# Kernel tuning notes

Measured on AMD Instinct MI355X. Metric: run time of the kernel, lower is better.

The kernel has to match this reference:

```python
import jax, jax.numpy as jnp
import numpy as np

KERNEL_SIZE = 5
SIGMA = 1.5
SIGMA_COLOR = 0.1
EPS = 1e-8


def _gaussian_kernel_2d(k, sigma):
    x = jnp.arange(k, dtype=jnp.float32) - k // 2
    k1 = jnp.exp(-0.5 * (x / sigma) ** 2)
    k1 = k1 / k1.sum()
    return jnp.outer(k1, k1)  # [k, k]


def setup_inputs() -> dict:
    key = jax.random.key(0)
    img = jax.random.uniform(key, (2, 3, 1024, 1024), dtype=jnp.float32)
    return {"img": img}


def reference(img):
    # Bilateral filter, faithful to Denoise._bilateral_filter.
    B, C, H, W = img.shape
    k = KERNEL_SIZE
    pad = k // 2
    k2 = _gaussian_kernel_2d(k, SIGMA).astype(img.dtype).reshape(-1)  # [k*k]

    img_padded = jnp.pad(img, ((0, 0), (0, 0), (pad, pad), (pad, pad)), mode='reflect')
    # patches: [B, C, H, W, k*k] via k*k shifted views (loop over fixed small window)
    patches = jnp.stack(
        [img_padded[:, :, i:i + H, j:j + W] for i in range(k) for j in range(k)],
        axis=-1,
    )
    center = img[..., None]
    intensity_diff = patches - center
    color_weights = jnp.exp(-0.5 * (intensity_diff / SIGMA_COLOR) ** 2)
    weights = color_weights * k2  # broadcast spatial gaussian over last axis
    weights_sum = weights.sum(axis=-1, keepdims=True) + EPS
    weights_normalized = weights / weights_sum
    img_filtered = (patches * weights_normalized).sum(axis=-1)
    return img_filtered
```

## Files before the change

kernel.cpp:

```cpp
#include <hip/hip_runtime.h>


#define TX 64
#define TY 64
#define BY 4
#define RPT (TY / BY)
#define PAD 2
#define LW (TX + 2 * PAD)
#define LH (TY + 2 * PAD)

#if __has_builtin(__builtin_amdgcn_exp2f)
#define EXP2(x) __builtin_amdgcn_exp2f(x)
#else
#define EXP2(x) exp2f(x)
#endif

__global__ __launch_bounds__(256) void bilateral_kernel(
    const float* __restrict__ in, float* __restrict__ out, int H, int W)
{
    const int z  = blockIdx.z;
    const int x0 = blockIdx.x * TX;
    const int y0 = blockIdx.y * TY;
    const int tx = threadIdx.x;
    const int ty = threadIdx.y;
    const int tid = ty * TX + tx;

    __shared__ float tile[LH * LW];
    const float* img = in + (size_t)z * H * W;

    for (int idx = tid; idx < LH * LW; idx += TX * BY) {
        int r = idx / LW;
        int c = idx - r * LW;
        int gy = y0 - PAD + r;
        int gx = x0 - PAD + c;
        gy = gy < 0 ? -gy : (gy >= H ? 2 * H - 2 - gy : gy);
        gx = gx < 0 ? -gx : (gx >= W ? 2 * W - 2 - gx : gx);
        tile[idx] = img[(size_t)gy * W + gx];
    }
    __syncthreads();

    float k1[5];
    float s = 0.f;
#pragma unroll
    for (int i = 0; i < 5; ++i) {
        float x = (float)(i - 2) * (1.0f / 1.5f);
        k1[i] = __expf(-0.5f * x * x);
        s += k1[i];
    }
    const float inv_s = 1.0f / s;
    float l1[5];
#pragma unroll
    for (int i = 0; i < 5; ++i) l1[i] = __log2f(k1[i] * inv_s);
    float lk2[5][5];
#pragma unroll
    for (int i = 0; i < 5; ++i)
#pragma unroll
        for (int j = 0; j < 5; ++j) lk2[i][j] = l1[i] + l1[j];
    const float K2C = EXP2(lk2[2][2]);
    const float S = 8.49321794f;

    const int ly0 = ty * RPT;

    float win[5][5];
#pragma unroll
    for (int r = 0; r < 4; ++r)
#pragma unroll
        for (int j = 0; j < 5; ++j)
            win[r][j] = tile[(ly0 + r) * LW + tx + j];

#pragma unroll
    for (int q = 0; q < RPT; ++q) {
        const int fill = (q + 4) % 5;
#pragma unroll
        for (int j = 0; j < 5; ++j)
            win[fill][j] = tile[(ly0 + q + 4) * LW + tx + j];

        const float ctr = win[(q + 2) % 5][2];
        float wsum = K2C;
        float vsum = K2C * ctr;
#pragma unroll
        for (int i = 0; i < 5; ++i) {
            const int ri = (q + i) % 5;
#pragma unroll
            for (int j = 0; j < 5; ++j) {
                if (i == 2 && j == 2) continue;
                const float p = win[ri][j];
                const float u = (p - ctr) * S;
                const float w = EXP2(__builtin_fmaf(-u, u, lk2[i][j]));
                wsum += w;
                vsum = __builtin_fmaf(w, p, vsum);
            }
        }
        const float r = __builtin_amdgcn_rcpf(wsum + 1e-8f);
        out[((size_t)z * H + (y0 + ly0 + q)) * W + (x0 + tx)] = vsum * r;
    }
}

extern "C" void kernel_launch(void* const* d_in, const int* in_sizes, int n_in,
                              void* d_out, int out_size, void* d_ws, size_t ws_size,
                              hipStream_t stream) {
    const float* img = (const float*)d_in[0];
    float* out = (float*)d_out;

    const int B = 2, C = 3, H = 1024, W = 1024;
    dim3 block(TX, BY, 1);
    dim3 grid(W / TX, H / TY, B * C);
    bilateral_kernel<<<grid, block, 0, stream>>>(img, out, H, W);
}
```

Measured before the change: 106.5 us.

## Process two output rows per iteration with pre-scaled tile and constant spatial weights

Halves the tile height to launch more blocks, pre-multiplies the shared tile by the color scale so the per-tap subtract-multiply becomes a single subtract, hard-codes the log2 spatial kernel constants, and computes two output rows per loop step with split accumulators to raise ILP. The final normalization folds the scale back in through an FMA. The change costs more registers per thread and more halo reloads per output because of the shorter tiles. An unused constant-memory dummy variable is also added.

```diff
diff --git a/kernel.cpp b/kernel.cpp
--- a/kernel.cpp
+++ b/kernel.cpp
@@ -2,7 +2,7 @@
 
 
 #define TX 64
-#define TY 64
+#define TY 32
 #define BY 4
 #define RPT (TY / BY)
 #define PAD 2
@@ -15,6 +15,8 @@
 #define EXP2(x) exp2f(x)
 #endif
 
+__device__ __constant__ const float d_dummy = 0.f;
+
 __global__ __launch_bounds__(256) void bilateral_kernel(
     const float* __restrict__ in, float* __restrict__ out, int H, int W)
 {
@@ -24,6 +26,9 @@
     const int tx = threadIdx.x;
     const int ty = threadIdx.y;
     const int tid = ty * TX + tx;
+
+    const float S    = 8.49321794f;
+    const float SEPS = 8.49321794e-8f;
 
     __shared__ float tile[LH * LW];
     const float* img = in + (size_t)z * H * W;
@@ -35,33 +40,17 @@
         int gx = x0 - PAD + c;
         gy = gy < 0 ? -gy : (gy >= H ? 2 * H - 2 - gy : gy);
         gx = gx < 0 ? -gx : (gx >= W ? 2 * W - 2 - gx : gx);
-        tile[idx] = img[(size_t)gy * W + gx];
+        tile[idx] = img[(size_t)gy * W + gx] * S;
     }
     __syncthreads();
 
-    float k1[5];
-    float s = 0.f;
-#pragma unroll
-    for (int i = 0; i < 5; ++i) {
-        float x = (float)(i - 2) * (1.0f / 1.5f);
-        k1[i] = __expf(-0.5f * x * x);
-        s += k1[i];
-    }
-    const float inv_s = 1.0f / s;
-    float l1[5];
-#pragma unroll
-    for (int i = 0; i < 5; ++i) l1[i] = __log2f(k1[i] * inv_s);
-    float lk2[5][5];
-#pragma unroll
-    for (int i = 0; i < 5; ++i)
-#pragma unroll
-        for (int j = 0; j < 5; ++j) lk2[i][j] = l1[i] + l1[j];
-    const float K2C = EXP2(lk2[2][2]);
-    const float S = 8.49321794f;
+    const float L[5] = {-3.0579510f, -2.0961485f, -1.7755560f,
+                        -2.0961485f, -3.0579510f};
+    const float K2C = 0.08531170f;
 
     const int ly0 = ty * RPT;
 
-    float win[5][5];
+    float win[6][5];
 #pragma unroll
     for (int r = 0; r < 4; ++r)
 #pragma unroll
@@ -69,30 +58,51 @@
             win[r][j] = tile[(ly0 + r) * LW + tx + j];
 
 #pragma unroll
-    for (int q = 0; q < RPT; ++q) {
-        const int fill = (q + 4) % 5;
+    for (int q = 0; q < RPT; q += 2) {
+        const int sA = (q + 4) % 6, sB = (q + 5) % 6;
 #pragma unroll
         for (int j = 0; j < 5; ++j)
-            win[fill][j] = tile[(ly0 + q + 4) * LW + tx + j];
+            win[sA][j] = tile[(ly0 + q + 4) * LW + tx + j];
+#pragma unroll
+        for (int j = 0; j < 5; ++j)
+            win[sB][j] = tile[(ly0 + q + 5) * LW + tx + j];
 
-        const float ctr = win[(q + 2) % 5][2];
-        float wsum = K2C;
-        float vsum = K2C * ctr;
+        const float c0 = win[(q + 2) % 6][2];
+        const float c1 = win[(q + 3) % 6][2];
+
+        float w0a = K2C, v0a = K2C * c0, w0b = 0.f, v0b = 0.f;
+        float w1a = K2C, v1a = K2C * c1, w1b = 0.f, v1b = 0.f;
+
 #pragma unroll
         for (int i = 0; i < 5; ++i) {
-            const int ri = (q + i) % 5;
+            const int r0 = (q + i) % 6;
+            const int r1 = (q + 1 + i) % 6;
 #pragma unroll
             for (int j = 0; j < 5; ++j) {
-                if (i == 2 && j == 2) continue;
-                const float p = win[ri][j];
-                const float u = (p - ctr) * S;
-                const float w = EXP2(__builtin_fmaf(-u, u, lk2[i][j]));
-                wsum += w;
-                vsum = __builtin_fmaf(w, p, vsum);
+                const float lk2 = L[i] + L[j];
+                if (!(i == 2 && j == 2)) {
+                    const float p = win[r0][j];
+                    const float u = p - c0;
+                    const float w = EXP2(__builtin_fmaf(-u, u, lk2));
+                    if (((i * 5 + j) & 1) == 0) { w0a += w; v0a = __builtin_fmaf(w, p, v0a); }
+                    else                        { w0b += w; v0b = __builtin_fmaf(w, p, v0b); }
+                }
+                if (!(i == 2 && j == 2)) {
+                    const float p = win[r1][j];
+                    const float u = p - c1;
+                    const float w = EXP2(__builtin_fmaf(-u, u, lk2));
+                    if (((i * 5 + j) & 1) == 0) { w1a += w; v1a = __builtin_fmaf(w, p, v1a); }
+                    else                        { w1b += w; v1b = __builtin_fmaf(w, p, v1b); }
+                }
             }
         }
-        const float r = __builtin_amdgcn_rcpf(wsum + 1e-8f);
-        out[((size_t)z * H + (y0 + ly0 + q)) * W + (x0 + tx)] = vsum * r;
+        const float w0 = w0a + w0b, v0 = v0a + v0b;
+        const float w1 = w1a + w1b, v1 = v1a + v1b;
+        const float r0v = __builtin_amdgcn_rcpf(__builtin_fmaf(S, w0, SEPS));
+        const float r1v = __builtin_amdgcn_rcpf(__builtin_fmaf(S, w1, SEPS));
+        const size_t base = ((size_t)z * H + (y0 + ly0 + q)) * W + (x0 + tx);
+        out[base]     = v0 * r0v;
+        out[base + W] = v1 * r1v;
     }
 }
 
```

After: 102.1 us. 4.1% less time.
